# Kernel optimization log

Hardware: AMD Instinct MI355X
Metric: run time of the kernel (lower is better)

Reference implementation:

```python
import jax, jax.numpy as jnp
import numpy as np

N = 50000
NODE_C = 256
HIDDEN = 128
EDGE_C = 128
E = 800000


def setup_inputs() -> dict:
    key = jax.random.key(0)
    k1, k2, k3, k4 = jax.random.split(key, 4)
    x = jax.random.normal(k1, (N, NODE_C), dtype=jnp.float32)
    edge_index = jax.random.randint(k2, (2, E), 0, N, dtype=jnp.int64)
    # nn.Linear default init ~ U(-1/sqrt(fan_in), 1/sqrt(fan_in)); biases zero per torch.nn.init.zeros_
    s1 = 1.0 / np.sqrt(NODE_C)
    W_proj = jax.random.uniform(k3, (NODE_C, 2 * HIDDEN), jnp.float32, -s1, s1)
    b_proj = jnp.zeros((2 * HIDDEN,), jnp.float32)
    s2 = 1.0 / np.sqrt(2 * HIDDEN)
    W_o = jax.random.uniform(k4, (2 * HIDDEN, EDGE_C), jnp.float32, -s2, s2)
    b_o = jnp.zeros((EDGE_C,), jnp.float32)
    return {"x": x, "edge_index": edge_index, "W_proj": W_proj, "b_proj": b_proj, "W_o": W_o, "b_o": b_o}


def reference(x, edge_index, W_proj, b_proj, W_o, b_o):
    # project nodes, split into q/k halves
    qk = x @ W_proj + b_proj            # [N, 2H]
    q, k = qk[:, :HIDDEN], qk[:, HIDDEN:]
    qe = q[edge_index[0]]               # [E, H] gather of source nodes
    ke = k[edge_index[1]]               # [E, H] gather of target nodes
    edge_attr = jnp.concatenate([qe * ke, qe - ke], axis=-1)  # [E, 2H]
    return edge_attr @ W_o + b_o        # [E, EDGE_C]
```

## Files before the change

### kernel.cpp

```cpp
#include <hip/hip_runtime.h>
#include <stdint.h>

typedef __attribute__((ext_vector_type(8))) __bf16 bf16x8;
typedef __attribute__((ext_vector_type(4))) float f32x4;
typedef __attribute__((ext_vector_type(8))) unsigned short u16x8;
typedef __attribute__((ext_vector_type(4))) unsigned short u16x4;

#define N_NODES 50000
#define N_EDGES 800000
#define C_IN    256
#define HID     128
#define C_OUT   128

__device__ __forceinline__ float bf2f(unsigned short u) {
  union { unsigned int u; float f; } c; c.u = ((unsigned int)u) << 16; return c.f;
}
__device__ __forceinline__ unsigned short f2bf(float f) {
  union { float f; unsigned int u; } c; c.f = f;
  unsigned int x = c.u + 0x7FFFu + ((c.u >> 16) & 1u);
  return (unsigned short)(x >> 16);
}

__global__ void k_idx(const int* __restrict__ raw, int* __restrict__ src,
                      int* __restrict__ dst) {
  int e = blockIdx.x * 256 + threadIdx.x;
  bool is64 = true;
  #pragma unroll
  for (int i = 0; i < 16; ++i) is64 = is64 && (raw[2*i+1] == 0);
  if (e < N_EDGES) {
    if (is64) {
      const long long* r = (const long long*)raw;
      src[e] = (int)r[e];
      dst[e] = (int)r[N_EDGES + e];
    } else {
      src[e] = raw[e];
      dst[e] = raw[N_EDGES + e];
    }
  }
}

__global__ void k_prep_w(const float* __restrict__ W, unsigned short* __restrict__ frag,
                         int Ncols) {
  int t = blockIdx.x * 256 + threadIdx.x;
  int total = 8 * (Ncols / 16) * 64 * 8;
  if (t >= total) return;
  int j    = t & 7;
  int lane = (t >> 3) & 63;
  int kk   = (t >> 9) & 7;
  int c    = t >> 12;
  int k    = kk * 32 + (lane >> 4) * 8 + j;
  int col  = c * 16 + (lane & 15);
  frag[t] = f2bf(W[(size_t)k * Ncols + col]);
}

__global__ __launch_bounds__(256) void k_node(
    const float* __restrict__ x, const unsigned short* __restrict__ wpf,
    const float* __restrict__ b_proj,
    unsigned short* __restrict__ qb, unsigned short* __restrict__ kb) {
  __shared__ unsigned short xs[64 * 264];
  int base = blockIdx.x * 64;
  int tid = threadIdx.x;
  #pragma unroll
  for (int it = 0; it < 16; ++it) {
    int idx = it * 256 + tid;
    int row = idx >> 6;
    int c4  = idx & 63;
    float4 v = make_float4(0.f, 0.f, 0.f, 0.f);
    if (base + row < N_NODES)
      v = *(const float4*)(x + (size_t)(base + row) * C_IN + c4 * 4);
    u16x4 u = { f2bf(v.x), f2bf(v.y), f2bf(v.z), f2bf(v.w) };
    *(u16x4*)&xs[row * 264 + c4 * 4] = u;
  }
  __syncthreads();
  int lane = tid & 63, w = tid >> 6;
  f32x4 acc[16];
  #pragma unroll
  for (int c = 0; c < 16; ++c) acc[c] = (f32x4){0.f, 0.f, 0.f, 0.f};
  int arow  = w * 16 + (lane & 15);
  int koffb = (lane >> 4) * 8;
  #pragma unroll
  for (int kk = 0; kk < 8; ++kk) {
    bf16x8 a = *(const bf16x8*)&xs[arow * 264 + kk * 32 + koffb];
    #pragma unroll
    for (int c = 0; c < 16; ++c) {
      bf16x8 b = *(const bf16x8*)(wpf + (((c * 8 + kk) * 64 + lane) << 3));
      acc[c] = __builtin_amdgcn_mfma_f32_16x16x32_bf16(a, b, acc[c], 0, 0, 0);
    }
  }
  int r0   = base + w * 16 + ((lane >> 4) << 2);
  int colb = lane & 15;
  #pragma unroll
  for (int c = 0; c < 16; ++c) {
    int col = c * 16 + colb;
    float bp = b_proj[col];
    #pragma unroll
    for (int j = 0; j < 4; ++j) {
      int row = r0 + j;
      if (row < N_NODES) {
        unsigned short h = f2bf(acc[c][j] + bp);
        if (col < HID) qb[(size_t)row * HID + col] = h;
        else           kb[(size_t)row * HID + col - HID] = h;
      }
    }
  }
}

__global__ __launch_bounds__(256, 4) void k_edge(
    const int* __restrict__ src, const int* __restrict__ dst,
    const unsigned short* __restrict__ qb, const unsigned short* __restrict__ kb,
    const unsigned short* __restrict__ wof, const float* __restrict__ b_o,
    float* __restrict__ out) {
  __shared__ unsigned short ea[64 * 264];
  int base = blockIdx.x * 64;
  int tid = threadIdx.x;
  int e = tid >> 2, q4 = tid & 3;
  int s = src[base + e], d = dst[base + e];
  const u16x8* qrow = (const u16x8*)(qb + (size_t)s * HID);
  const u16x8* krow = (const u16x8*)(kb + (size_t)d * HID);
  #pragma unroll
  for (int i = 0; i < 4; ++i) {
    int c8 = q4 * 4 + i;
    u16x8 q8 = qrow[c8];
    u16x8 k8 = krow[c8];
    u16x8 p8, m8;
    #pragma unroll
    for (int j = 0; j < 8; ++j) {
      float qf = bf2f(q8[j]), kf = bf2f(k8[j]);
      p8[j] = f2bf(qf * kf);
      m8[j] = f2bf(qf - kf);
    }
    *(u16x8*)&ea[e * 264 + c8 * 8]       = p8;
    *(u16x8*)&ea[e * 264 + 128 + c8 * 8] = m8;
  }
  __syncthreads();
  int lane = tid & 63, w = tid >> 6;
  f32x4 acc[8];
  #pragma unroll
  for (int c = 0; c < 8; ++c) acc[c] = (f32x4){0.f, 0.f, 0.f, 0.f};
  int arow  = w * 16 + (lane & 15);
  int koffb = (lane >> 4) * 8;
  #pragma unroll
  for (int kk = 0; kk < 8; ++kk) {
    bf16x8 a = *(const bf16x8*)&ea[arow * 264 + kk * 32 + koffb];
    #pragma unroll
    for (int c = 0; c < 8; ++c) {
      bf16x8 b = *(const bf16x8*)(wof + (((c * 8 + kk) * 64 + lane) << 3));
      acc[c] = __builtin_amdgcn_mfma_f32_16x16x32_bf16(a, b, acc[c], 0, 0, 0);
    }
  }
  int r0   = base + w * 16 + ((lane >> 4) << 2);
  int colb = lane & 15;
  #pragma unroll
  for (int c = 0; c < 8; ++c) {
    int col = c * 16 + colb;
    float bo = b_o[col];
    #pragma unroll
    for (int j = 0; j < 4; ++j) {
      out[(size_t)(r0 + j) * C_OUT + col] = acc[c][j] + bo;
    }
  }
}

extern "C" void kernel_launch(void* const* d_in, const int* in_sizes, int n_in,
                              void* d_out, int out_size, void* d_ws, size_t ws_size,
                              hipStream_t stream) {
  const float* x      = (const float*)d_in[0];
  const int*   eidx   = (const int*)d_in[1];
  const float* W_proj = (const float*)d_in[2];
  const float* b_proj = (const float*)d_in[3];
  const float* W_o    = (const float*)d_in[4];
  const float* b_o    = (const float*)d_in[5];
  float* out = (float*)d_out;

  char* ws = (char*)d_ws;
  int* src = (int*)ws;                        ws += (size_t)N_EDGES * 4;
  int* dst = (int*)ws;                        ws += (size_t)N_EDGES * 4;
  unsigned short* qb  = (unsigned short*)ws;  ws += (size_t)N_NODES * HID * 2;
  unsigned short* kb  = (unsigned short*)ws;  ws += (size_t)N_NODES * HID * 2;
  unsigned short* wof = (unsigned short*)ws;  ws += 8 * 8 * 64 * 8 * 2;
  unsigned short* wpf = (unsigned short*)ws;  ws += 16 * 8 * 64 * 8 * 2;

  k_idx<<<dim3((N_EDGES + 255) / 256), dim3(256), 0, stream>>>(eidx, src, dst);
  k_prep_w<<<dim3((8 * 8 * 64 * 8 + 255) / 256), dim3(256), 0, stream>>>(W_o, wof, C_OUT);
  k_prep_w<<<dim3((16 * 8 * 64 * 8 + 255) / 256), dim3(256), 0, stream>>>(W_proj, wpf, 256);
  k_node<<<dim3((N_NODES + 63) / 64), dim3(256), 0, stream>>>(x, wpf, b_proj, qb, kb);
  k_edge<<<dim3(N_EDGES / 64), dim3(256), 0, stream>>>(src, dst, qb, kb, wof, b_o, out);
}
```

Measured before the change: 625.6 us.

## Make edge kernel persistent with register-resident weights and prefetched gathers

The edge kernel becomes persistent with 1024 blocks looping over 64-edge tiles. Each warp keeps its 32-column slice of the W_o fragments in registers instead of reloading them per tile. The next tile's index and q/k gather is issued before the MFMA phase, with double-buffered LDS. The separate index-conversion kernel is removed and int64/int32 indices are read directly. The cost is higher register use, and with a single barrier per iteration the double buffering relies on the buffer alternation to stay safe.

```diff
diff --git a/kernel.cpp b/kernel.cpp
--- a/kernel.cpp
+++ b/kernel.cpp
@@ -11,6 +11,9 @@
 #define C_IN    256
 #define HID     128
 #define C_OUT   128
+#define NT      (N_EDGES / 64)
+#define NBLK_E  1024
+#define EA_STRIDE 264
 
 __device__ __forceinline__ float bf2f(unsigned short u) {
   union { unsigned int u; float f; } c; c.u = ((unsigned int)u) << 16; return c.f;
@@ -19,24 +22,6 @@
   union { float f; unsigned int u; } c; c.f = f;
   unsigned int x = c.u + 0x7FFFu + ((c.u >> 16) & 1u);
   return (unsigned short)(x >> 16);
-}
-
-__global__ void k_idx(const int* __restrict__ raw, int* __restrict__ src,
-                      int* __restrict__ dst) {
-  int e = blockIdx.x * 256 + threadIdx.x;
-  bool is64 = true;
-  #pragma unroll
-  for (int i = 0; i < 16; ++i) is64 = is64 && (raw[2*i+1] == 0);
-  if (e < N_EDGES) {
-    if (is64) {
-      const long long* r = (const long long*)raw;
-      src[e] = (int)r[e];
-      dst[e] = (int)r[N_EDGES + e];
-    } else {
-      src[e] = raw[e];
-      dst[e] = raw[N_EDGES + e];
-    }
-  }
 }
 
 __global__ void k_prep_w(const float* __restrict__ W, unsigned short* __restrict__ frag,
@@ -57,7 +42,7 @@
     const float* __restrict__ x, const unsigned short* __restrict__ wpf,
     const float* __restrict__ b_proj,
     unsigned short* __restrict__ qb, unsigned short* __restrict__ kb) {
-  __shared__ unsigned short xs[64 * 264];
+  __shared__ unsigned short xs[64 * EA_STRIDE];
   int base = blockIdx.x * 64;
   int tid = threadIdx.x;
   #pragma unroll
@@ -69,7 +54,7 @@
     if (base + row < N_NODES)
       v = *(const float4*)(x + (size_t)(base + row) * C_IN + c4 * 4);
     u16x4 u = { f2bf(v.x), f2bf(v.y), f2bf(v.z), f2bf(v.w) };
-    *(u16x4*)&xs[row * 264 + c4 * 4] = u;
+    *(u16x4*)&xs[row * EA_STRIDE + c4 * 4] = u;
   }
   __syncthreads();
   int lane = tid & 63, w = tid >> 6;
@@ -80,7 +65,7 @@
   int koffb = (lane >> 4) * 8;
   #pragma unroll
   for (int kk = 0; kk < 8; ++kk) {
-    bf16x8 a = *(const bf16x8*)&xs[arow * 264 + kk * 32 + koffb];
+    bf16x8 a = *(const bf16x8*)&xs[arow * EA_STRIDE + kk * 32 + koffb];
     #pragma unroll
     for (int c = 0; c < 16; ++c) {
       bf16x8 b = *(const bf16x8*)(wpf + (((c * 8 + kk) * 64 + lane) << 3));
@@ -105,59 +90,98 @@
   }
 }
 
-__global__ __launch_bounds__(256, 4) void k_edge(
-    const int* __restrict__ src, const int* __restrict__ dst,
+__global__ __launch_bounds__(256) void k_edge(
+    const int* __restrict__ eraw,
     const unsigned short* __restrict__ qb, const unsigned short* __restrict__ kb,
     const unsigned short* __restrict__ wof, const float* __restrict__ b_o,
     float* __restrict__ out) {
-  __shared__ unsigned short ea[64 * 264];
-  int base = blockIdx.x * 64;
-  int tid = threadIdx.x;
-  int e = tid >> 2, q4 = tid & 3;
-  int s = src[base + e], d = dst[base + e];
-  const u16x8* qrow = (const u16x8*)(qb + (size_t)s * HID);
-  const u16x8* krow = (const u16x8*)(kb + (size_t)d * HID);
-  #pragma unroll
-  for (int i = 0; i < 4; ++i) {
-    int c8 = q4 * 4 + i;
-    u16x8 q8 = qrow[c8];
-    u16x8 k8 = krow[c8];
-    u16x8 p8, m8;
-    #pragma unroll
-    for (int j = 0; j < 8; ++j) {
-      float qf = bf2f(q8[j]), kf = bf2f(k8[j]);
-      p8[j] = f2bf(qf * kf);
-      m8[j] = f2bf(qf - kf);
-    }
-    *(u16x8*)&ea[e * 264 + c8 * 8]       = p8;
-    *(u16x8*)&ea[e * 264 + 128 + c8 * 8] = m8;
-  }
-  __syncthreads();
-  int lane = tid & 63, w = tid >> 6;
-  f32x4 acc[8];
-  #pragma unroll
-  for (int c = 0; c < 8; ++c) acc[c] = (f32x4){0.f, 0.f, 0.f, 0.f};
-  int arow  = w * 16 + (lane & 15);
-  int koffb = (lane >> 4) * 8;
-  #pragma unroll
-  for (int kk = 0; kk < 8; ++kk) {
-    bf16x8 a = *(const bf16x8*)&ea[arow * 264 + kk * 32 + koffb];
-    #pragma unroll
-    for (int c = 0; c < 8; ++c) {
-      bf16x8 b = *(const bf16x8*)(wof + (((c * 8 + kk) * 64 + lane) << 3));
-      acc[c] = __builtin_amdgcn_mfma_f32_16x16x32_bf16(a, b, acc[c], 0, 0, 0);
-    }
-  }
-  int r0   = base + w * 16 + ((lane >> 4) << 2);
-  int colb = lane & 15;
-  #pragma unroll
-  for (int c = 0; c < 8; ++c) {
-    int col = c * 16 + colb;
-    float bo = b_o[col];
-    #pragma unroll
-    for (int j = 0; j < 4; ++j) {
-      out[(size_t)(r0 + j) * C_OUT + col] = acc[c][j] + bo;
-    }
+  __shared__ unsigned short ea[2][64 * EA_STRIDE];
+  const int tid   = threadIdx.x;
+  const int lane  = tid & 63, w = tid >> 6;
+  const int e_loc = tid >> 2, q4 = tid & 3;
+
+  bool is64 = true;
+  #pragma unroll
+  for (int i = 0; i < 16; ++i) is64 = is64 && (eraw[2 * i + 1] == 0);
+  const long long* e64 = (const long long*)eraw;
+
+  bf16x8 bfr[2][8];
+  #pragma unroll
+  for (int ct = 0; ct < 2; ++ct)
+    #pragma unroll
+    for (int kk = 0; kk < 8; ++kk)
+      bfr[ct][kk] = *(const bf16x8*)(wof + ((((w * 2 + ct) * 8 + kk) * 64 + lane) << 3));
+  const float bo0 = b_o[w * 32 + (lane & 15)];
+  const float bo1 = b_o[w * 32 + 16 + (lane & 15)];
+
+  u16x8 qv[4], kv[4];
+  int t = blockIdx.x;
+  if (t < NT) {
+    int ge = t * 64 + e_loc;
+    int s, d;
+    if (is64) { s = (int)e64[ge]; d = (int)e64[N_EDGES + ge]; }
+    else      { s = eraw[ge];     d = eraw[N_EDGES + ge]; }
+    const u16x8* qrow = (const u16x8*)(qb + (size_t)s * HID);
+    const u16x8* krow = (const u16x8*)(kb + (size_t)d * HID);
+    #pragma unroll
+    for (int i = 0; i < 4; ++i) { qv[i] = qrow[q4 * 4 + i]; kv[i] = krow[q4 * 4 + i]; }
+  }
+
+  int buf = 0;
+  for (; t < NT; t += NBLK_E) {
+    unsigned short* eb = &ea[buf][0];
+    #pragma unroll
+    for (int i = 0; i < 4; ++i) {
+      int c8 = q4 * 4 + i;
+      u16x8 p8, m8;
+      #pragma unroll
+      for (int j = 0; j < 8; ++j) {
+        float qf = bf2f(qv[i][j]), kf = bf2f(kv[i][j]);
+        p8[j] = f2bf(qf * kf);
+        m8[j] = f2bf(qf - kf);
+      }
+      *(u16x8*)&eb[e_loc * EA_STRIDE + c8 * 8]       = p8;
+      *(u16x8*)&eb[e_loc * EA_STRIDE + 128 + c8 * 8] = m8;
+    }
+    int tn = t + NBLK_E;
+    if (tn < NT) {
+      int ge = tn * 64 + e_loc;
+      int s, d;
+      if (is64) { s = (int)e64[ge]; d = (int)e64[N_EDGES + ge]; }
+      else      { s = eraw[ge];     d = eraw[N_EDGES + ge]; }
+      const u16x8* qrow = (const u16x8*)(qb + (size_t)s * HID);
+      const u16x8* krow = (const u16x8*)(kb + (size_t)d * HID);
+      #pragma unroll
+      for (int i = 0; i < 4; ++i) { qv[i] = qrow[q4 * 4 + i]; kv[i] = krow[q4 * 4 + i]; }
+    }
+    __syncthreads();
+    f32x4 acc[4][2];
+    #pragma unroll
+    for (int et = 0; et < 4; ++et) {
+      acc[et][0] = (f32x4){0.f, 0.f, 0.f, 0.f};
+      acc[et][1] = (f32x4){0.f, 0.f, 0.f, 0.f};
+    }
+    const int arow_off = (lane & 15) * EA_STRIDE + (lane >> 4) * 8;
+    #pragma unroll
+    for (int kk = 0; kk < 8; ++kk) {
+      #pragma unroll
+      for (int et = 0; et < 4; ++et) {
+        bf16x8 a = *(const bf16x8*)&eb[et * 16 * EA_STRIDE + arow_off + kk * 32];
+        acc[et][0] = __builtin_amdgcn_mfma_f32_16x16x32_bf16(a, bfr[0][kk], acc[et][0], 0, 0, 0);
+        acc[et][1] = __builtin_amdgcn_mfma_f32_16x16x32_bf16(a, bfr[1][kk], acc[et][1], 0, 0, 0);
+      }
+    }
+    #pragma unroll
+    for (int et = 0; et < 4; ++et) {
+      int r0 = t * 64 + et * 16 + ((lane >> 4) << 2);
+      #pragma unroll
+      for (int j = 0; j < 4; ++j) {
+        float* op = out + (size_t)(r0 + j) * C_OUT + w * 32 + (lane & 15);
+        op[0]  = acc[et][0][j] + bo0;
+        op[16] = acc[et][1][j] + bo1;
+      }
+    }
+    buf ^= 1;
   }
 }
 
@@ -173,16 +197,13 @@
   float* out = (float*)d_out;
 
   char* ws = (char*)d_ws;
-  int* src = (int*)ws;                        ws += (size_t)N_EDGES * 4;
-  int* dst = (int*)ws;                        ws += (size_t)N_EDGES * 4;
   unsigned short* qb  = (unsigned short*)ws;  ws += (size_t)N_NODES * HID * 2;
   unsigned short* kb  = (unsigned short*)ws;  ws += (size_t)N_NODES * HID * 2;
   unsigned short* wof = (unsigned short*)ws;  ws += 8 * 8 * 64 * 8 * 2;
   unsigned short* wpf = (unsigned short*)ws;  ws += 16 * 8 * 64 * 8 * 2;
 
-  k_idx<<<dim3((N_EDGES + 255) / 256), dim3(256), 0, stream>>>(eidx, src, dst);
   k_prep_w<<<dim3((8 * 8 * 64 * 8 + 255) / 256), dim3(256), 0, stream>>>(W_o, wof, C_OUT);
   k_prep_w<<<dim3((16 * 8 * 64 * 8 + 255) / 256), dim3(256), 0, stream>>>(W_proj, wpf, 256);
   k_node<<<dim3((N_NODES + 63) / 64), dim3(256), 0, stream>>>(x, wpf, b_proj, qb, kb);
-  k_edge<<<dim3(N_EDGES / 64), dim3(256), 0, stream>>>(src, dst, qb, kb, wof, b_o, out);
-}
+  k_edge<<<dim3(NBLK_E), dim3(256), 0, stream>>>(eidx, qb, kb, wof, b_o, out);
+}
```

Measured after the change: 600.6 us. 1.04x faster.
